# Performance work log

Measured on AMD Instinct MI355X. Metric: run time of the kernel, lower is better.

## Reference

```python
import jax, jax.numpy as jnp
import numpy as np

N_NODES = 50000
N_EDGES = 1600000
N_GRAPHS = 64
DIM_IN, DIM_H, HEADS, DIM_OUT = 128, 32, 2, 64
NEG_SLOPE = 0.2


def _segment_softmax(scores, seg, num_segments):
    # scores: [E, H], seg: [E] int -> softmax over edges sharing the same dst
    m = jax.ops.segment_max(scores, seg, num_segments=num_segments)
    m = jnp.where(jnp.isfinite(m), m, 0.0)  # empty segments -> -inf; neutralize
    e = jnp.exp(scores - m[seg])
    s = jax.ops.segment_sum(e, seg, num_segments=num_segments)
    return e / (s[seg] + 1e-16)


def gatv2_conv(x, edge_index, Wl, Wr, att, bias, heads, ch, n_nodes):
    # PyG GATv2Conv defaults: add_self_loops=True, share_weights=False, concat heads.
    loops = jnp.arange(n_nodes, dtype=edge_index.dtype)
    ei = jnp.concatenate([edge_index, jnp.stack([loops, loops])], axis=1)
    src, dst = ei[0], ei[1]
    xl = (x @ Wl).reshape(n_nodes, heads, ch)  # source transform
    xr = (x @ Wr).reshape(n_nodes, heads, ch)  # target transform
    el = xl[src]                               # [E+N, H, C] gather
    s = jax.nn.leaky_relu(el + xr[dst], NEG_SLOPE)
    scores = jnp.einsum('ehc,hc->eh', s, att)  # [E+N, H]
    alpha = _segment_softmax(scores, dst, n_nodes)
    out = jax.ops.segment_sum(alpha[..., None] * el, dst, num_segments=n_nodes)
    return out.reshape(n_nodes, heads * ch) + bias


def setup_inputs() -> dict:
    key = jax.random.key(0)
    ks = jax.random.split(key, 12)
    glorot = lambda k, shp: jax.random.normal(k, shp, jnp.float32) * np.sqrt(2.0 / (shp[0] + shp[-1]))
    x = jax.random.normal(ks[0], (N_NODES, DIM_IN), jnp.float32)
    edge_index = jax.random.randint(ks[1], (2, N_EDGES), 0, N_NODES, jnp.int64)
    batch = jnp.sort(jax.random.randint(ks[2], (N_NODES,), 0, N_GRAPHS, jnp.int64))
    H1 = DIM_H * HEADS
    return {
        'x': x, 'edge_index': edge_index, 'batch': batch,
        'Wl1': glorot(ks[3], (DIM_IN, H1)), 'Wr1': glorot(ks[4], (DIM_IN, H1)),
        'att1': glorot(ks[5], (HEADS, DIM_H)), 'b1': jnp.zeros((H1,), jnp.float32),
        'Wl2': glorot(ks[6], (H1, DIM_OUT)), 'Wr2': glorot(ks[7], (H1, DIM_OUT)),
        'att2': glorot(ks[8], (1, DIM_OUT)), 'b2': jnp.zeros((DIM_OUT,), jnp.float32),
        'lin_w': glorot(ks[9], (DIM_OUT, 2)), 'lin_b': jnp.zeros((2,), jnp.float32),
    }


def reference(x, edge_index, batch, Wl1, Wr1, att1, b1, Wl2, Wr2, att2, b2, lin_w, lin_b):
    # eval mode: dropout is identity
    h = gatv2_conv(x, edge_index, Wl1, Wr1, att1, b1, HEADS, DIM_H, N_NODES)
    h = jax.nn.elu(h)
    h = jax.nn.elu(gatv2_conv(h, edge_index, Wl2, Wr2, att2, b2, 1, DIM_OUT, N_NODES))
    # global mean pool over graphs
    sums = jax.ops.segment_sum(h, batch, num_segments=N_GRAPHS)
    cnts = jax.ops.segment_sum(jnp.ones((N_NODES,), h.dtype), batch, num_segments=N_GRAPHS)
    pooled = sums / jnp.maximum(cnts, 1.0)[:, None]
    return pooled @ lin_w + lin_b
```

## Files before the change

### kernel.cpp

```cpp
#include <hip/hip_runtime.h>
#include <hip/hip_bf16.h>
#include <math.h>

#define N_NODES 50000
#define N_EDGES 1600000
#define N_GRAPHS 64
#define NB 391
#define NBLK 256
#define CHUNK 6250
#define ROW_STRIDE 80
#define SENT 50047

typedef unsigned int u32;

__device__ __forceinline__ float bcf(u32 u) { return __builtin_bit_cast(float, u); }

template <int CTRL>
__device__ __forceinline__ float dpp_add(float v) {
    int r = __builtin_amdgcn_update_dpp(0, __builtin_bit_cast(int, v), CTRL, 0xF, 0xF, true);
    return v + __builtin_bit_cast(float, r);
}

__device__ __forceinline__ u32 pack_bf16x2(float lo, float hi) {
    unsigned short l = __builtin_bit_cast(unsigned short, __float2bfloat16(lo));
    unsigned short h = __builtin_bit_cast(unsigned short, __float2bfloat16(hi));
    return (u32)l | ((u32)h << 16);
}

template <int K, bool FUSE_COUNT>
__global__ __launch_bounds__(256) void gemm_tiled(
    const float* __restrict__ x, const float* __restrict__ Wl,
    const float* __restrict__ Wr, const float* __restrict__ att,
    u32* __restrict__ xlb, float* __restrict__ xr,
    float* __restrict__ alb, float* __restrict__ arb,
    const int* __restrict__ ei, int* __restrict__ countsRM, int gemmBlocks) {
    __shared__ float xs[64][K + 1];
    const int t = threadIdx.x;
    if (FUSE_COUNT && blockIdx.x >= gemmBlocks) {
        int* h = (int*)&xs[0][0];
        const int cb = blockIdx.x - gemmBlocks;
        for (int k = t; k < NB; k += 256) h[k] = 0;
        __syncthreads();
        const int base = cb * CHUNK;
        for (int e = base + t; e < base + CHUNK; e += 256)
            atomicAdd(&h[ei[N_EDGES + e] >> 7], 1);
        __syncthreads();
        for (int k = t; k < NB; k += 256) countsRM[cb * NB + k] = h[k];
        return;
    }
    const int base = blockIdx.x * 64;
    const int nf4 = 64 * K / 4;
    for (int f = t; f < nf4; f += 256) {
        const int row = f / (K / 4);
        const int c4 = f % (K / 4);
        float4 v = make_float4(0.f, 0.f, 0.f, 0.f);
        if (base + row < N_NODES)
            v = *(const float4*)(x + (size_t)(base + row) * K + c4 * 4);
        xs[row][c4 * 4 + 0] = v.x;
        xs[row][c4 * 4 + 1] = v.y;
        xs[row][c4 * 4 + 2] = v.z;
        xs[row][c4 * 4 + 3] = v.w;
    }
    __syncthreads();
    const int lane = t & 63;
    const int w = __builtin_amdgcn_readfirstlane(t >> 6);
    const float* __restrict__ W = (w < 2) ? Wl : Wr;
    const int cb = (w & 1) * 32;
    float acc[32];
#pragma unroll
    for (int j = 0; j < 32; ++j) acc[j] = 0.f;
#pragma unroll 2
    for (int k = 0; k < K; ++k) {
        const float xv = xs[lane][k];
        const float* __restrict__ Wrow = W + k * 64 + cb;
#pragma unroll
        for (int j = 0; j < 32; ++j) acc[j] = fmaf(xv, Wrow[j], acc[j]);
    }
    const int n = base + lane;
    if (n < N_NODES) {
        float av = 0.f;
#pragma unroll
        for (int j = 0; j < 32; ++j) av = fmaf(att[cb + j], acc[j], av);
        if (w < 2) {
            alb[(size_t)n * 2 + (w & 1)] = av;
            u32 pk[16];
#pragma unroll
            for (int j = 0; j < 32; j += 2) pk[j >> 1] = pack_bf16x2(acc[j], acc[j + 1]);
            uint4* dst = (uint4*)(xlb + (size_t)n * 32 + (w & 1) * 16);
#pragma unroll
            for (int j = 0; j < 4; ++j)
                dst[j] = make_uint4(pk[j * 4], pk[j * 4 + 1], pk[j * 4 + 2], pk[j * 4 + 3]);
        } else {
            arb[(size_t)n * 2 + (w & 1)] = av;
#pragma unroll
            for (int j = 0; j < 32; j += 4) {
                float4 v = {acc[j], acc[j + 1], acc[j + 2], acc[j + 3]};
                *(float4*)(xr + (size_t)n * 64 + cb + j) = v;
            }
        }
    }
}

__global__ __launch_bounds__(256) void scan_bucket(
    const int* __restrict__ countsRM, int* __restrict__ scanT,
    int* __restrict__ totals) {
    __shared__ int tmp[256];
    const int b = blockIdx.x;
    const int t = threadIdx.x;
    const int v0 = countsRM[t * NB + b];
    tmp[t] = v0;
    __syncthreads();
    for (int off = 1; off < 256; off <<= 1) {
        int v = (t >= off) ? tmp[t - off] : 0;
        __syncthreads();
        tmp[t] += v;
        __syncthreads();
    }
    scanT[b * 256 + t] = tmp[t] - v0;
    if (t == 255) totals[b] = tmp[t];
}

__global__ __launch_bounds__(512) void scan_total(
    const int* __restrict__ totals, int* __restrict__ bucketBase,
    float* __restrict__ alb) {
    __shared__ int tmp[512];
    const int t = threadIdx.x;
    const int v0 = (t < NB) ? totals[t] : 0;
    tmp[t] = v0;
    __syncthreads();
    for (int off = 1; off < 512; off <<= 1) {
        int v = (t >= off) ? tmp[t - off] : 0;
        __syncthreads();
        tmp[t] += v;
        __syncthreads();
    }
    if (t < NB) bucketBase[t] = tmp[t] - v0;
    if (t == NB - 1) bucketBase[NB] = tmp[t];
    if (t == 0) { alb[(size_t)SENT * 2] = -1e30f; alb[(size_t)SENT * 2 + 1] = -1e30f; }
}

__global__ __launch_bounds__(256) void scatter2_kernel(
    const int* __restrict__ ei, const int* __restrict__ scanT,
    const int* __restrict__ bucketBase, int* __restrict__ sortedE) {
    __shared__ int cursor[NB];
    const int t = threadIdx.x;
    const int b = blockIdx.x;
    for (int k = t; k < NB; k += 256)
        cursor[k] = bucketBase[k] + scanT[k * 256 + b];
    __syncthreads();
    const int base = b * CHUNK;
    for (int e = base + t; e < base + CHUNK; e += 256) {
        const int s = ei[e];
        const int d = ei[N_EDGES + e];
        const int idx = atomicAdd(&cursor[d >> 7], 1);
        sortedE[idx] = (s << 7) | (d & 127);
    }
}

__global__ __launch_bounds__(256) void expand_kernel(
    const int* __restrict__ bucketBase, const int* __restrict__ sortedE,
    int* __restrict__ deg, int* __restrict__ rows) {
    __shared__ int ldeg[128];
    const int b = blockIdx.x;
    const int t = threadIdx.x;
    const int node_base = b * 128;
    if (t < 128) {
        const int n = node_base + t;
        ldeg[t] = 1;
        if (n < N_NODES) rows[(size_t)n * ROW_STRIDE] = n;
    }
    __syncthreads();
    const int beg = bucketBase[b];
    const int end = bucketBase[b + 1];
    for (int i = beg + t; i < end; i += 256) {
        const int en = sortedE[i];
        const int ld = en & 127;
        const int pos = atomicAdd(&ldeg[ld], 1);
        if (pos < ROW_STRIDE) rows[(size_t)(node_base + ld) * ROW_STRIDE + pos] = en >> 7;
    }
    __syncthreads();
    if (t < 128) {
        const int n = node_base + t;
        if (n < N_NODES) {
            int c = ldeg[t];
            c = c < ROW_STRIDE ? c : ROW_STRIDE;
            const int cp = (c + 7) & ~7;
            for (int j = c; j < cp; ++j) rows[(size_t)n * ROW_STRIDE + j] = SENT;
            deg[n] = cp;
        }
    }
}

template <bool L1>
__global__ __launch_bounds__(256) void node_layer(
    const int* __restrict__ deg, const int* __restrict__ rows,
    const u32* __restrict__ xlb, const float* __restrict__ xr,
    const float* __restrict__ alb, const float* __restrict__ arb,
    const float* __restrict__ att, const float* __restrict__ bias,
    float* __restrict__ hout) {
    const int n = (blockIdx.x * 256 + threadIdx.x) >> 6;
    const int lane = threadIdx.x & 63;
    const int sub = lane & 7;
    const int g = lane >> 3;
    const float4 xra = *(const float4*)(xr + (size_t)n * 64 + sub * 8);
    const float4 xrb = *(const float4*)(xr + (size_t)n * 64 + sub * 8 + 4);
    const float4 ata = *(const float4*)(att + sub * 8);
    const float4 atb = *(const float4*)(att + sub * 8 + 4);
    const float2 ar2 = *(const float2*)(arb + (size_t)n * 2);
    const float based = 0.6f * (L1 ? ((sub & 4) ? ar2.y : ar2.x) : (ar2.x + ar2.y));

    float c0 = 0.f, c1 = 0.f, c2 = 0.f, c3 = 0.f;
    float c4 = 0.f, c5 = 0.f, c6 = 0.f, c7 = 0.f;
    float ssum = 0.f;
    const int cp = __builtin_amdgcn_readfirstlane(deg[n]);
    const int* __restrict__ row = rows + (size_t)n * ROW_STRIDE;
    for (int i = 0; i < cp; i += 8) {
        const int s = row[i + g];
        float als;
        if (L1) {
            als = alb[(size_t)s * 2 + ((sub >> 2) & 1)];
        } else {
            const float2 a2 = *(const float2*)(alb + (size_t)s * 2);
            als = a2.x + a2.y;
        }
        const uint4 r4 = *(const uint4*)(xlb + (size_t)s * 32 + sub * 4);
        const float a0 = bcf(r4.x << 16), a1 = bcf(r4.x & 0xFFFF0000u);
        const float a2f = bcf(r4.y << 16), a3 = bcf(r4.y & 0xFFFF0000u);
        const float a4 = bcf(r4.z << 16), a5 = bcf(r4.z & 0xFFFF0000u);
        const float a6 = bcf(r4.w << 16), a7 = bcf(r4.w & 0xFFFF0000u);
        float v = ata.x * fabsf(a0 + xra.x);
        v = fmaf(ata.y, fabsf(a1 + xra.y), v);
        v = fmaf(ata.z, fabsf(a2f + xra.z), v);
        v = fmaf(ata.w, fabsf(a3 + xra.w), v);
        v = fmaf(atb.x, fabsf(a4 + xrb.x), v);
        v = fmaf(atb.y, fabsf(a5 + xrb.y), v);
        v = fmaf(atb.z, fabsf(a6 + xrb.z), v);
        v = fmaf(atb.w, fabsf(a7 + xrb.w), v);
        v = dpp_add<0xB1>(v);
        v = dpp_add<0x4E>(v);
        if (!L1) v = dpp_add<0x141>(v);
        const float ev = __expf(fmaf(0.6f, als, fmaf(0.4f, v, based)));
        c0 = fmaf(ev, a0, c0); c1 = fmaf(ev, a1, c1);
        c2 = fmaf(ev, a2f, c2); c3 = fmaf(ev, a3, c3);
        c4 = fmaf(ev, a4, c4); c5 = fmaf(ev, a5, c5);
        c6 = fmaf(ev, a6, c6); c7 = fmaf(ev, a7, c7);
        ssum += ev;
    }
#define XRED(x) x += __shfl_xor(x, 8); x += __shfl_xor(x, 16); x += __shfl_xor(x, 32);
    XRED(c0) XRED(c1) XRED(c2) XRED(c3) XRED(c4) XRED(c5) XRED(c6) XRED(c7) XRED(ssum)
#undef XRED
    if (g == 0) {
        const float inv = 1.f / (ssum + 1e-16f);
        const float4 ba = *(const float4*)(bias + sub * 8);
        const float4 bb = *(const float4*)(bias + sub * 8 + 4);
        float o[8] = {c0 * inv + ba.x, c1 * inv + ba.y, c2 * inv + ba.z, c3 * inv + ba.w,
                      c4 * inv + bb.x, c5 * inv + bb.y, c6 * inv + bb.z, c7 * inv + bb.w};
#pragma unroll
        for (int j = 0; j < 8; ++j) o[j] = o[j] > 0.f ? o[j] : expm1f(o[j]);
        *(float4*)(hout + (size_t)n * 64 + sub * 8) = make_float4(o[0], o[1], o[2], o[3]);
        *(float4*)(hout + (size_t)n * 64 + sub * 8 + 4) = make_float4(o[4], o[5], o[6], o[7]);
    }
}

__global__ __launch_bounds__(64) void pool_kernel(
    const float* __restrict__ h2, const int* __restrict__ batch,
    float* __restrict__ pooled, float* __restrict__ cnt) {
    const int t = threadIdx.x;
    const int base = blockIdx.x * 64;
    float local = 0.f, lc = 0.f;
    int cur = -1;
    for (int j = 0; j < 64; ++j) {
        const int n = base + j;
        if (n >= N_NODES) break;
        const int g = batch[n];
        if (g != cur) {
            if (cur >= 0) {
                unsafeAtomicAdd(&pooled[cur * 64 + t], local);
                if (t == 0) unsafeAtomicAdd(&cnt[cur], lc);
            }
            cur = g; local = 0.f; lc = 0.f;
        }
        local += h2[n * 64 + t];
        lc += 1.f;
    }
    if (cur >= 0) {
        unsafeAtomicAdd(&pooled[cur * 64 + t], local);
        if (t == 0) unsafeAtomicAdd(&cnt[cur], lc);
    }
}

__global__ __launch_bounds__(128) void head_kernel(
    const float* __restrict__ pooled, const float* __restrict__ cnt,
    const float* __restrict__ lin_w, const float* __restrict__ lin_b,
    float* __restrict__ out) {
    const int i = threadIdx.x;
    const int g = i >> 1, k = i & 1;
    float c = cnt[g];
    c = c > 1.f ? c : 1.f;
    float a = 0.f;
#pragma unroll
    for (int j = 0; j < 64; ++j) a = fmaf(pooled[g * 64 + j] / c, lin_w[j * 2 + k], a);
    out[i] = a + lin_b[k];
}

extern "C" void kernel_launch(void* const* d_in, const int* in_sizes, int n_in,
                              void* d_out, int out_size, void* d_ws, size_t ws_size,
                              hipStream_t stream) {
    const float* x     = (const float*)d_in[0];
    const int*   ei    = (const int*)d_in[1];
    const int*   batch = (const int*)d_in[2];
    const float* Wl1   = (const float*)d_in[3];
    const float* Wr1   = (const float*)d_in[4];
    const float* att1  = (const float*)d_in[5];
    const float* b1    = (const float*)d_in[6];
    const float* Wl2   = (const float*)d_in[7];
    const float* Wr2   = (const float*)d_in[8];
    const float* att2  = (const float*)d_in[9];
    const float* b2    = (const float*)d_in[10];
    const float* lin_w = (const float*)d_in[11];
    const float* lin_b = (const float*)d_in[12];

    float* ws = (float*)d_ws;
    u32*   xlb      = (u32*)ws;
    float* xr       = ws + 1601536;
    float* h1       = ws + 4801536;
    float* alb      = ws + 8001536;
    float* arb      = ws + 8101632;
    int*   rows     = (int*)(ws + 8201728);
    int*   deg      = (int*)(ws + 12205568);
    int*   countsRM = (int*)(ws + 12255616);
    int*   scanT    = (int*)(ws + 12355712);
    int*   totals   = (int*)(ws + 12455808);
    int*   bb       = (int*)(ws + 12456320);
    float* pooled   = ws + 12456832;
    float* cnt      = ws + 12460928;
    int*   sortedE  = (int*)(ws + 12460992);

    hipMemsetAsync(pooled, 0, (size_t)(4096 + 64) * sizeof(float), stream);

    const int gblocks = (N_NODES + 63) / 64;

    gemm_tiled<128, true><<<gblocks + NBLK, 256, 0, stream>>>(
        x, Wl1, Wr1, att1, xlb, xr, alb, arb, ei, countsRM, gblocks);

    scan_bucket<<<NB, 256, 0, stream>>>(countsRM, scanT, totals);
    scan_total<<<1, 512, 0, stream>>>(totals, bb, alb);
    scatter2_kernel<<<NBLK, 256, 0, stream>>>(ei, scanT, bb, sortedE);
    expand_kernel<<<NB, 256, 0, stream>>>(bb, sortedE, deg, rows);

    node_layer<true><<<N_NODES / 4, 256, 0, stream>>>(
        deg, rows, xlb, xr, alb, arb, att1, b1, h1);

    gemm_tiled<64, false><<<gblocks, 256, 0, stream>>>(
        h1, Wl2, Wr2, att2, xlb, xr, alb, arb, nullptr, nullptr, gblocks);
    node_layer<false><<<N_NODES / 4, 256, 0, stream>>>(
        deg, rows, xlb, xr, alb, arb, att2, b2, h1);

    pool_kernel<<<(N_NODES + 63) / 64, 64, 0, stream>>>(h1, batch, pooled, cnt);
    head_kernel<<<1, 128, 0, stream>>>(pooled, cnt, lin_w, lin_b, (float*)d_out);
}
```

Baseline: 311.4 us.

## Fuse edge scatter into layer-1 GEMM and pre-sum layer-2 attention scalars

Edge counting moves to its own kernel, and the heavier bucket scatter now runs as extra blocks of the layer-1 GEMM launch, so atomics-bound scatter work overlaps the GEMM instead of the lighter count. The GEMM stages x through shared memory in 64-column chunks, which shrinks the LDS tile for K=128 and may raise occupancy. Layer 2 now stores a single pre-summed source attention scalar per node, so the neighbour loop does one scalar load instead of a float2 load plus an add. In exchange there is one more kernel launch and an extra barrier in the layer-2 GEMM epilogue.

```diff
diff --git a/kernel.cpp b/kernel.cpp
--- a/kernel.cpp
+++ b/kernel.cpp
@@ -27,41 +27,84 @@
     return (u32)l | ((u32)h << 16);
 }
 
-template <int K, bool FUSE_COUNT>
+__global__ __launch_bounds__(256) void count_kernel(
+    const int* __restrict__ ei, int* __restrict__ countsRM) {
+    __shared__ int h[NB];
+    const int t = threadIdx.x;
+    for (int k = t; k < NB; k += 256) h[k] = 0;
+    __syncthreads();
+    const int base = blockIdx.x * CHUNK;
+    for (int e = base + t; e < base + CHUNK; e += 256)
+        atomicAdd(&h[ei[N_EDGES + e] >> 7], 1);
+    __syncthreads();
+    for (int k = t; k < NB; k += 256) countsRM[blockIdx.x * NB + k] = h[k];
+}
+
+__global__ __launch_bounds__(256) void scan_bucket(
+    const int* __restrict__ countsRM, int* __restrict__ scanT,
+    int* __restrict__ totals) {
+    __shared__ int tmp[256];
+    const int b = blockIdx.x;
+    const int t = threadIdx.x;
+    const int v0 = countsRM[t * NB + b];
+    tmp[t] = v0;
+    __syncthreads();
+    for (int off = 1; off < 256; off <<= 1) {
+        int v = (t >= off) ? tmp[t - off] : 0;
+        __syncthreads();
+        tmp[t] += v;
+        __syncthreads();
+    }
+    scanT[b * 256 + t] = tmp[t] - v0;
+    if (t == 255) totals[b] = tmp[t];
+}
+
+__global__ __launch_bounds__(512) void scan_total(
+    const int* __restrict__ totals, int* __restrict__ bucketBase,
+    float* __restrict__ alb) {
+    __shared__ int tmp[512];
+    const int t = threadIdx.x;
+    const int v0 = (t < NB) ? totals[t] : 0;
+    tmp[t] = v0;
+    __syncthreads();
+    for (int off = 1; off < 512; off <<= 1) {
+        int v = (t >= off) ? tmp[t - off] : 0;
+        __syncthreads();
+        tmp[t] += v;
+        __syncthreads();
+    }
+    if (t < NB) bucketBase[t] = tmp[t] - v0;
+    if (t == NB - 1) bucketBase[NB] = tmp[t];
+    if (t == 0) { alb[(size_t)SENT * 2] = -1e30f; alb[(size_t)SENT * 2 + 1] = -1e30f; }
+}
+
+template <int K, bool FUSE_SCATTER>
 __global__ __launch_bounds__(256) void gemm_tiled(
     const float* __restrict__ x, const float* __restrict__ Wl,
     const float* __restrict__ Wr, const float* __restrict__ att,
     u32* __restrict__ xlb, float* __restrict__ xr,
     float* __restrict__ alb, float* __restrict__ arb,
-    const int* __restrict__ ei, int* __restrict__ countsRM, int gemmBlocks) {
-    __shared__ float xs[64][K + 1];
-    const int t = threadIdx.x;
-    if (FUSE_COUNT && blockIdx.x >= gemmBlocks) {
-        int* h = (int*)&xs[0][0];
-        const int cb = blockIdx.x - gemmBlocks;
-        for (int k = t; k < NB; k += 256) h[k] = 0;
-        __syncthreads();
-        const int base = cb * CHUNK;
-        for (int e = base + t; e < base + CHUNK; e += 256)
-            atomicAdd(&h[ei[N_EDGES + e] >> 7], 1);
-        __syncthreads();
-        for (int k = t; k < NB; k += 256) countsRM[cb * NB + k] = h[k];
+    const int* __restrict__ ei, const int* __restrict__ scanT,
+    const int* __restrict__ bb, int* __restrict__ sortedE, int gemmBlocks) {
+    __shared__ float xs[64][65];
+    __shared__ float als[64];
+    const int t = threadIdx.x;
+    if (FUSE_SCATTER && blockIdx.x >= gemmBlocks) {
+        int* cursor = (int*)&xs[0][0];
+        const int b = blockIdx.x - gemmBlocks;
+        for (int k = t; k < NB; k += 256)
+            cursor[k] = bb[k] + scanT[k * 256 + b];
+        __syncthreads();
+        const int base = b * CHUNK;
+        for (int e = base + t; e < base + CHUNK; e += 256) {
+            const int s = ei[e];
+            const int d = ei[N_EDGES + e];
+            const int idx = atomicAdd(&cursor[d >> 7], 1);
+            sortedE[idx] = (s << 7) | (d & 127);
+        }
         return;
     }
     const int base = blockIdx.x * 64;
-    const int nf4 = 64 * K / 4;
-    for (int f = t; f < nf4; f += 256) {
-        const int row = f / (K / 4);
-        const int c4 = f % (K / 4);
-        float4 v = make_float4(0.f, 0.f, 0.f, 0.f);
-        if (base + row < N_NODES)
-            v = *(const float4*)(x + (size_t)(base + row) * K + c4 * 4);
-        xs[row][c4 * 4 + 0] = v.x;
-        xs[row][c4 * 4 + 1] = v.y;
-        xs[row][c4 * 4 + 2] = v.z;
-        xs[row][c4 * 4 + 3] = v.w;
-    }
-    __syncthreads();
     const int lane = t & 63;
     const int w = __builtin_amdgcn_readfirstlane(t >> 6);
     const float* __restrict__ W = (w < 2) ? Wl : Wr;
@@ -69,20 +112,43 @@
     float acc[32];
 #pragma unroll
     for (int j = 0; j < 32; ++j) acc[j] = 0.f;
+#pragma unroll
+    for (int c = 0; c < K / 64; ++c) {
+        if (c) __syncthreads();
+        for (int f = t; f < 1024; f += 256) {
+            const int row = f >> 4;
+            const int c4 = f & 15;
+            float4 v = make_float4(0.f, 0.f, 0.f, 0.f);
+            if (base + row < N_NODES)
+                v = *(const float4*)(x + (size_t)(base + row) * K + c * 64 + c4 * 4);
+            xs[row][c4 * 4 + 0] = v.x;
+            xs[row][c4 * 4 + 1] = v.y;
+            xs[row][c4 * 4 + 2] = v.z;
+            xs[row][c4 * 4 + 3] = v.w;
+        }
+        __syncthreads();
 #pragma unroll 2
-    for (int k = 0; k < K; ++k) {
-        const float xv = xs[lane][k];
-        const float* __restrict__ Wrow = W + k * 64 + cb;
-#pragma unroll
-        for (int j = 0; j < 32; ++j) acc[j] = fmaf(xv, Wrow[j], acc[j]);
+        for (int kk = 0; kk < 64; ++kk) {
+            const float xv = xs[lane][kk];
+            const float* __restrict__ Wrow = W + (c * 64 + kk) * 64 + cb;
+#pragma unroll
+            for (int j = 0; j < 32; ++j) acc[j] = fmaf(xv, Wrow[j], acc[j]);
+        }
     }
     const int n = base + lane;
+    float av = 0.f;
+#pragma unroll
+    for (int j = 0; j < 32; ++j) av = fmaf(att[cb + j], acc[j], av);
+    if (K == 64) {
+        if (w == 0) als[lane] = av;
+        __syncthreads();
+        if (w == 1 && n < N_NODES) alb[n] = als[lane] + av;
+        if (blockIdx.x == 0 && t == 0) alb[SENT] = -1e30f;
+    } else {
+        if (w < 2 && n < N_NODES) alb[(size_t)n * 2 + (w & 1)] = av;
+    }
     if (n < N_NODES) {
-        float av = 0.f;
-#pragma unroll
-        for (int j = 0; j < 32; ++j) av = fmaf(att[cb + j], acc[j], av);
         if (w < 2) {
-            alb[(size_t)n * 2 + (w & 1)] = av;
             u32 pk[16];
 #pragma unroll
             for (int j = 0; j < 32; j += 2) pk[j >> 1] = pack_bf16x2(acc[j], acc[j + 1]);
@@ -98,62 +164,6 @@
                 *(float4*)(xr + (size_t)n * 64 + cb + j) = v;
             }
         }
-    }
-}
-
-__global__ __launch_bounds__(256) void scan_bucket(
-    const int* __restrict__ countsRM, int* __restrict__ scanT,
-    int* __restrict__ totals) {
-    __shared__ int tmp[256];
-    const int b = blockIdx.x;
-    const int t = threadIdx.x;
-    const int v0 = countsRM[t * NB + b];
-    tmp[t] = v0;
-    __syncthreads();
-    for (int off = 1; off < 256; off <<= 1) {
-        int v = (t >= off) ? tmp[t - off] : 0;
-        __syncthreads();
-        tmp[t] += v;
-        __syncthreads();
-    }
-    scanT[b * 256 + t] = tmp[t] - v0;
-    if (t == 255) totals[b] = tmp[t];
-}
-
-__global__ __launch_bounds__(512) void scan_total(
-    const int* __restrict__ totals, int* __restrict__ bucketBase,
-    float* __restrict__ alb) {
-    __shared__ int tmp[512];
-    const int t = threadIdx.x;
-    const int v0 = (t < NB) ? totals[t] : 0;
-    tmp[t] = v0;
-    __syncthreads();
-    for (int off = 1; off < 512; off <<= 1) {
-        int v = (t >= off) ? tmp[t - off] : 0;
-        __syncthreads();
-        tmp[t] += v;
-        __syncthreads();
-    }
-    if (t < NB) bucketBase[t] = tmp[t] - v0;
-    if (t == NB - 1) bucketBase[NB] = tmp[t];
-    if (t == 0) { alb[(size_t)SENT * 2] = -1e30f; alb[(size_t)SENT * 2 + 1] = -1e30f; }
-}
-
-__global__ __launch_bounds__(256) void scatter2_kernel(
-    const int* __restrict__ ei, const int* __restrict__ scanT,
-    const int* __restrict__ bucketBase, int* __restrict__ sortedE) {
-    __shared__ int cursor[NB];
-    const int t = threadIdx.x;
-    const int b = blockIdx.x;
-    for (int k = t; k < NB; k += 256)
-        cursor[k] = bucketBase[k] + scanT[k * 256 + b];
-    __syncthreads();
-    const int base = b * CHUNK;
-    for (int e = base + t; e < base + CHUNK; e += 256) {
-        const int s = ei[e];
-        const int d = ei[N_EDGES + e];
-        const int idx = atomicAdd(&cursor[d >> 7], 1);
-        sortedE[idx] = (s << 7) | (d & 127);
     }
 }
 
@@ -216,13 +226,7 @@
     const int* __restrict__ row = rows + (size_t)n * ROW_STRIDE;
     for (int i = 0; i < cp; i += 8) {
         const int s = row[i + g];
-        float als;
-        if (L1) {
-            als = alb[(size_t)s * 2 + ((sub >> 2) & 1)];
-        } else {
-            const float2 a2 = *(const float2*)(alb + (size_t)s * 2);
-            als = a2.x + a2.y;
-        }
+        const float als = L1 ? alb[(size_t)s * 2 + ((sub >> 2) & 1)] : alb[s];
         const uint4 r4 = *(const uint4*)(xlb + (size_t)s * 32 + sub * 4);
         const float a0 = bcf(r4.x << 16), a1 = bcf(r4.x & 0xFFFF0000u);
         const float a2f = bcf(r4.y << 16), a3 = bcf(r4.y & 0xFFFF0000u);
@@ -340,19 +344,20 @@
 
     const int gblocks = (N_NODES + 63) / 64;
 
-    gemm_tiled<128, true><<<gblocks + NBLK, 256, 0, stream>>>(
-        x, Wl1, Wr1, att1, xlb, xr, alb, arb, ei, countsRM, gblocks);
-
+    count_kernel<<<NBLK, 256, 0, stream>>>(ei, countsRM);
     scan_bucket<<<NB, 256, 0, stream>>>(countsRM, scanT, totals);
     scan_total<<<1, 512, 0, stream>>>(totals, bb, alb);
-    scatter2_kernel<<<NBLK, 256, 0, stream>>>(ei, scanT, bb, sortedE);
+
+    gemm_tiled<128, true><<<gblocks + NBLK, 256, 0, stream>>>(
+        x, Wl1, Wr1, att1, xlb, xr, alb, arb, ei, scanT, bb, sortedE, gblocks);
+
     expand_kernel<<<NB, 256, 0, stream>>>(bb, sortedE, deg, rows);
 
     node_layer<true><<<N_NODES / 4, 256, 0, stream>>>(
         deg, rows, xlb, xr, alb, arb, att1, b1, h1);
 
     gemm_tiled<64, false><<<gblocks, 256, 0, stream>>>(
-        h1, Wl2, Wr2, att2, xlb, xr, alb, arb, nullptr, nullptr, gblocks);
+        h1, Wl2, Wr2, att2, xlb, xr, alb, arb, nullptr, nullptr, nullptr, nullptr, gblocks);
     node_layer<false><<<N_NODES / 4, 256, 0, stream>>>(
         deg, rows, xlb, xr, alb, arb, att2, b2, h1);
 
```

Result: faster. 302.8 us (-2.8%).
